# Kernel optimization log

Hardware: AMD Instinct MI355X
Metric: run time of the kernel (lower is better)

The kernel has to match this reference:

```python
import jax, jax.numpy as jnp
import numpy as np

D_IN, D_OUT, RANK, N = 4096, 4096, 16, 8192


def _quantize_weight(w, bits):
    # round-to-nearest fake quantization, stored back as floats (as in the torch code)
    absmax = jnp.abs(w).max()
    scale = (2 ** (bits - 1) - 1) / absmax
    q = jnp.clip(jnp.round(w * scale), -2 ** (bits - 1), 2 ** (bits - 1) - 1)
    return q / scale


def _double_quantization(w, bits):
    absmax = jnp.abs(w).max()
    c1 = (2 ** (bits - 1) - 1) / absmax          # scalar fp32 scale
    q = jnp.clip(jnp.round(w * c1), -2 ** (bits - 1), 2 ** (bits - 1) - 1)
    return c1, q / c1                             # c_kbit_2 has same shape as w


def setup_inputs() -> dict:
    key = jax.random.key(0)
    kX, kW, kL1, kL2 = jax.random.split(key, 4)
    X = jax.random.normal(kX, (N, D_IN), dtype=jnp.float32)
    W0 = jax.random.normal(kW, (D_IN, D_OUT), dtype=jnp.float32)
    W_nf4 = _quantize_weight(W0, bits=4)
    c_fp32_1, c_kbit_2 = _double_quantization(W_nf4, bits=8)
    L1 = jax.random.normal(kL1, (D_IN, RANK), dtype=jnp.float32)
    L2 = jax.random.normal(kL2, (RANK, D_OUT), dtype=jnp.float32)
    return {"X": X, "W_nf4": W_nf4, "c_fp32_1": c_fp32_1,
            "c_kbit_2": c_kbit_2, "L1": L1, "L2": L2}


def reference(X, W_nf4, c_fp32_1, c_kbit_2, L1, L2):
    # dequantize: elementwise scalar * elementwise-tensor scaling of stored weight
    W = W_nf4 * c_fp32_1 * c_kbit_2               # [D_IN, D_OUT]
    # main GEMM + low-rank LoRA path, added in the epilogue
    Y = X @ W + (X @ L1) @ L2                     # [N, D_OUT]
    return Y
```

## Files before the change

kernel.cpp:

```cpp
#include <hip/hip_runtime.h>


#define M_ROWS 8192
#define K_DIM  4096
#define N_OUT  4096

typedef float  f32x4  __attribute__((ext_vector_type(4)));
typedef __bf16 bf16x8 __attribute__((ext_vector_type(8)));
typedef unsigned short ushort8v __attribute__((ext_vector_type(8)));

__device__ __forceinline__ unsigned short f2bf(float f) {
    __bf16 h = (__bf16)f;
    union { __bf16 h; unsigned short u; } v; v.h = h;
    return v.u;
}

__global__ __launch_bounds__(256) void cvt_x_kernel(const float* __restrict__ X,
                                                    ushort8v* __restrict__ Xh) {
    size_t tid = (size_t)blockIdx.x * 256 + threadIdx.x;
    const float4* xp = (const float4*)X;
    float4 a = xp[tid * 2];
    float4 b = xp[tid * 2 + 1];
    ushort8v o;
    o[0] = f2bf(a.x); o[1] = f2bf(a.y); o[2] = f2bf(a.z); o[3] = f2bf(a.w);
    o[4] = f2bf(b.x); o[5] = f2bf(b.y); o[6] = f2bf(b.z); o[7] = f2bf(b.w);
    Xh[tid] = o;
}

__global__ __launch_bounds__(256) void prep_w_kernel(
        const float* __restrict__ Wnf4, const float* __restrict__ c1p,
        const float* __restrict__ c2,   const float* __restrict__ L1,
        const float* __restrict__ L2,   unsigned short* __restrict__ Wt) {
    __shared__ float tile[64][65];
    __shared__ float sL2[16][64];
    __shared__ float sL1[64][16];
    const int t  = threadIdx.x;
    const int n0 = blockIdx.x * 64;
    const int k0 = blockIdx.y * 64;
    const float c1 = *c1p;

    {
        int r = t >> 4, c4 = (t & 15) * 4;
        *(float4*)&sL2[r][c4] = *(const float4*)&L2[(size_t)r * N_OUT + n0 + c4];
        int r1 = t >> 2, c1v = (t & 3) * 4;
        *(float4*)&sL1[r1][c1v] = *(const float4*)&L1[(size_t)(k0 + r1) * 16 + c1v];
    }
    __syncthreads();

    #pragma unroll
    for (int i = 0; i < 4; ++i) {
        int idx = i * 1024 + t * 4;
        int kk = idx >> 6, nn = idx & 63;
        size_t g = (size_t)(k0 + kk) * N_OUT + n0 + nn;
        float4 w = *(const float4*)&Wnf4[g];
        float4 s = *(const float4*)&c2[g];
        float o0 = w.x * c1 * s.x, o1 = w.y * c1 * s.y;
        float o2 = w.z * c1 * s.z, o3 = w.w * c1 * s.w;
        #pragma unroll
        for (int r = 0; r < 16; ++r) {
            float a = sL1[kk][r];
            o0 += a * sL2[r][nn];     o1 += a * sL2[r][nn + 1];
            o2 += a * sL2[r][nn + 2]; o3 += a * sL2[r][nn + 3];
        }
        tile[kk][nn] = o0; tile[kk][nn + 1] = o1;
        tile[kk][nn + 2] = o2; tile[kk][nn + 3] = o3;
    }
    __syncthreads();

    #pragma unroll
    for (int i = 0; i < 2; ++i) {
        int task = i * 256 + t;
        int kg = task & 7, nn = task >> 3;
        ushort8v o;
        #pragma unroll
        for (int j = 0; j < 8; ++j) o[j] = f2bf(tile[kg * 8 + j][nn]);
        *(ushort8v*)&Wt[(size_t)(n0 + nn) * K_DIM + k0 + kg * 8] = o;
    }
}

__global__ __launch_bounds__(256) void gemm_bt_kernel(
        const __bf16* __restrict__ A, const __bf16* __restrict__ Bt,
        float* __restrict__ C) {
    __shared__ __bf16 As[128 * 32];
    __shared__ __bf16 Bs[128 * 32];

    const int t    = threadIdx.x;
    const int w    = t >> 6;
    const int lane = t & 63;
    const int quad = lane >> 4;
    const int l16  = lane & 15;
    const int m0   = blockIdx.y * 128;
    const int n0   = blockIdx.x * 128;
    const int wm   = (w >> 1) * 64;
    const int wn   = (w & 1) * 64;

    const int srow = lane >> 2;
    const int scol = ((lane & 3) ^ ((lane >> 3) & 3)) * 8;
    const int rsw = (l16 >> 1) & 3;

    f32x4 acc[4][4] = {};

    for (int kb = 0; kb < K_DIM; kb += 32) {
        __syncthreads();
        #pragma unroll
        for (int j = 0; j < 2; ++j) {
            int row = w * 32 + j * 16 + srow;
            const __bf16* gp = A + (size_t)(m0 + row) * K_DIM + kb + scol;
            __builtin_amdgcn_global_load_lds(
                (const __attribute__((address_space(1))) unsigned int*)gp,
                (__attribute__((address_space(3))) unsigned int*)(As + (w * 32 + j * 16) * 32),
                16, 0, 0);
        }
        #pragma unroll
        for (int j = 0; j < 2; ++j) {
            int row = w * 32 + j * 16 + srow;
            const __bf16* gp = Bt + (size_t)(n0 + row) * K_DIM + kb + scol;
            __builtin_amdgcn_global_load_lds(
                (const __attribute__((address_space(1))) unsigned int*)gp,
                (__attribute__((address_space(3))) unsigned int*)(Bs + (w * 32 + j * 16) * 32),
                16, 0, 0);
        }
        __syncthreads();

        bf16x8 af[4], bf[4];
        #pragma unroll
        for (int i = 0; i < 4; ++i)
            af[i] = *(const bf16x8*)(As + (wm + i * 16 + l16) * 32 + ((quad ^ rsw) * 8));
        #pragma unroll
        for (int i = 0; i < 4; ++i)
            bf[i] = *(const bf16x8*)(Bs + (wn + i * 16 + l16) * 32 + ((quad ^ rsw) * 8));

        #pragma unroll
        for (int mt = 0; mt < 4; ++mt)
            #pragma unroll
            for (int nt = 0; nt < 4; ++nt)
                acc[mt][nt] = __builtin_amdgcn_mfma_f32_16x16x32_bf16(
                    af[mt], bf[nt], acc[mt][nt], 0, 0, 0);
    }

    #pragma unroll
    for (int mt = 0; mt < 4; ++mt) {
        int row = m0 + wm + mt * 16 + quad * 4;
        #pragma unroll
        for (int nt = 0; nt < 4; ++nt) {
            int col = n0 + wn + nt * 16 + l16;
            float* cp = C + (size_t)row * N_OUT + col;
            #pragma unroll
            for (int r = 0; r < 4; ++r)
                cp[(size_t)r * N_OUT] = acc[mt][nt][r];
        }
    }
}

extern "C" void kernel_launch(void* const* d_in, const int* in_sizes, int n_in,
                              void* d_out, int out_size, void* d_ws, size_t ws_size,
                              hipStream_t stream) {
    const float* X    = (const float*)d_in[0];
    const float* Wnf4 = (const float*)d_in[1];
    const float* c1   = (const float*)d_in[2];
    const float* c2   = (const float*)d_in[3];
    const float* L1   = (const float*)d_in[4];
    const float* L2   = (const float*)d_in[5];
    float* Y = (float*)d_out;

    unsigned short* Xh = (unsigned short*)d_ws;
    unsigned short* Wt = (unsigned short*)((char*)d_ws + (size_t)M_ROWS * K_DIM * 2);

    cvt_x_kernel<<<(M_ROWS * K_DIM / 8 + 255) / 256, 256, 0, stream>>>(X, (ushort8v*)Xh);
    prep_w_kernel<<<dim3(N_OUT / 64, K_DIM / 64), 256, 0, stream>>>(Wnf4, c1, c2, L1, L2, Wt);
    gemm_bt_kernel<<<dim3(N_OUT / 128, M_ROWS / 128), 256, 0, stream>>>(
        (const __bf16*)Xh, (const __bf16*)Wt, Y);
}
```

Baseline: 737.0 us.

## Switch GEMM to 32x32x16 MFMA tiles and merge prep kernels into one launch

The GEMM inner loop now issues 32x32x16 bf16 MFMAs on 2x2 accumulator tiles per wave instead of 16x16x32 MFMAs on 4x4 tiles. The fragment loads from shared memory and the output row mapping are rewritten to match. Separately, the X conversion and weight preparation kernels are merged into one launch that picks its branch by block index. The intent is fewer MFMA issues and LDS reads per k-step and one less kernel launch, at the cost of a larger per-instruction latency and a more scattered epilogue store pattern.

```diff
diff --git a/kernel.cpp b/kernel.cpp
--- a/kernel.cpp
+++ b/kernel.cpp
@@ -4,8 +4,10 @@
 #define M_ROWS 8192
 #define K_DIM  4096
 #define N_OUT  4096
+#define CVT_BLOCKS 16384
+#define PREPW_BLOCKS 4096
 
-typedef float  f32x4  __attribute__((ext_vector_type(4)));
+typedef float  f32x16 __attribute__((ext_vector_type(16)));
 typedef __bf16 bf16x8 __attribute__((ext_vector_type(8)));
 typedef unsigned short ushort8v __attribute__((ext_vector_type(8)));
 
@@ -15,28 +17,31 @@
     return v.u;
 }
 
-__global__ __launch_bounds__(256) void cvt_x_kernel(const float* __restrict__ X,
-                                                    ushort8v* __restrict__ Xh) {
-    size_t tid = (size_t)blockIdx.x * 256 + threadIdx.x;
-    const float4* xp = (const float4*)X;
-    float4 a = xp[tid * 2];
-    float4 b = xp[tid * 2 + 1];
-    ushort8v o;
-    o[0] = f2bf(a.x); o[1] = f2bf(a.y); o[2] = f2bf(a.z); o[3] = f2bf(a.w);
-    o[4] = f2bf(b.x); o[5] = f2bf(b.y); o[6] = f2bf(b.z); o[7] = f2bf(b.w);
-    Xh[tid] = o;
-}
-
-__global__ __launch_bounds__(256) void prep_w_kernel(
+__global__ __launch_bounds__(256) void prep_kernel(
+        const float* __restrict__ X,    ushort8v* __restrict__ Xh,
         const float* __restrict__ Wnf4, const float* __restrict__ c1p,
         const float* __restrict__ c2,   const float* __restrict__ L1,
         const float* __restrict__ L2,   unsigned short* __restrict__ Wt) {
     __shared__ float tile[64][65];
     __shared__ float sL2[16][64];
     __shared__ float sL1[64][16];
-    const int t  = threadIdx.x;
-    const int n0 = blockIdx.x * 64;
-    const int k0 = blockIdx.y * 64;
+    const int t = threadIdx.x;
+
+    if (blockIdx.x < CVT_BLOCKS) {
+        size_t tid = (size_t)blockIdx.x * 256 + t;
+        const float4* xp = (const float4*)X;
+        float4 a = xp[tid * 2];
+        float4 b = xp[tid * 2 + 1];
+        ushort8v o;
+        o[0] = f2bf(a.x); o[1] = f2bf(a.y); o[2] = f2bf(a.z); o[3] = f2bf(a.w);
+        o[4] = f2bf(b.x); o[5] = f2bf(b.y); o[6] = f2bf(b.z); o[7] = f2bf(b.w);
+        Xh[tid] = o;
+        return;
+    }
+
+    const int wb = blockIdx.x - CVT_BLOCKS;
+    const int n0 = (wb & 63) * 64;
+    const int k0 = (wb >> 6) * 64;
     const float c1 = *c1p;
 
     {
@@ -87,8 +92,8 @@
     const int t    = threadIdx.x;
     const int w    = t >> 6;
     const int lane = t & 63;
-    const int quad = lane >> 4;
-    const int l16  = lane & 15;
+    const int half = lane >> 5;
+    const int l32  = lane & 31;
     const int m0   = blockIdx.y * 128;
     const int n0   = blockIdx.x * 128;
     const int wm   = (w >> 1) * 64;
@@ -96,9 +101,9 @@
 
     const int srow = lane >> 2;
     const int scol = ((lane & 3) ^ ((lane >> 3) & 3)) * 8;
-    const int rsw = (l16 >> 1) & 3;
+    const int rsw = (l32 >> 1) & 3;
 
-    f32x4 acc[4][4] = {};
+    f32x16 acc[2][2] = {};
 
     for (int kb = 0; kb < K_DIM; kb += 32) {
         __syncthreads();
@@ -122,34 +127,45 @@
         }
         __syncthreads();
 
-        bf16x8 af[4], bf[4];
+        bf16x8 af[2][2], bf[2][2];
         #pragma unroll
-        for (int i = 0; i < 4; ++i)
-            af[i] = *(const bf16x8*)(As + (wm + i * 16 + l16) * 32 + ((quad ^ rsw) * 8));
+        for (int mt = 0; mt < 2; ++mt)
+            #pragma unroll
+            for (int ks = 0; ks < 2; ++ks) {
+                int row = wm + mt * 32 + l32;
+                int slot = (2 * ks + half) ^ rsw;
+                af[mt][ks] = *(const bf16x8*)(As + row * 32 + slot * 8);
+            }
         #pragma unroll
-        for (int i = 0; i < 4; ++i)
-            bf[i] = *(const bf16x8*)(Bs + (wn + i * 16 + l16) * 32 + ((quad ^ rsw) * 8));
+        for (int nt = 0; nt < 2; ++nt)
+            #pragma unroll
+            for (int ks = 0; ks < 2; ++ks) {
+                int row = wn + nt * 32 + l32;
+                int slot = (2 * ks + half) ^ rsw;
+                bf[nt][ks] = *(const bf16x8*)(Bs + row * 32 + slot * 8);
+            }
 
         #pragma unroll
-        for (int mt = 0; mt < 4; ++mt)
+        for (int ks = 0; ks < 2; ++ks)
             #pragma unroll
-            for (int nt = 0; nt < 4; ++nt)
-                acc[mt][nt] = __builtin_amdgcn_mfma_f32_16x16x32_bf16(
-                    af[mt], bf[nt], acc[mt][nt], 0, 0, 0);
+            for (int mt = 0; mt < 2; ++mt)
+                #pragma unroll
+                for (int nt = 0; nt < 2; ++nt)
+                    acc[mt][nt] = __builtin_amdgcn_mfma_f32_32x32x16_bf16(
+                        af[mt][ks], bf[nt][ks], acc[mt][nt], 0, 0, 0);
     }
 
     #pragma unroll
-    for (int mt = 0; mt < 4; ++mt) {
-        int row = m0 + wm + mt * 16 + quad * 4;
+    for (int mt = 0; mt < 2; ++mt)
         #pragma unroll
-        for (int nt = 0; nt < 4; ++nt) {
-            int col = n0 + wn + nt * 16 + l16;
-            float* cp = C + (size_t)row * N_OUT + col;
+        for (int nt = 0; nt < 2; ++nt) {
+            int col = n0 + wn + nt * 32 + l32;
             #pragma unroll
-            for (int r = 0; r < 4; ++r)
-                cp[(size_t)r * N_OUT] = acc[mt][nt][r];
+            for (int reg = 0; reg < 16; ++reg) {
+                int row = m0 + wm + mt * 32 + (reg & 3) + 8 * (reg >> 2) + 4 * half;
+                C[(size_t)row * N_OUT + col] = acc[mt][nt][reg];
+            }
         }
-    }
 }
 
 extern "C" void kernel_launch(void* const* d_in, const int* in_sizes, int n_in,
@@ -166,8 +182,8 @@
     unsigned short* Xh = (unsigned short*)d_ws;
     unsigned short* Wt = (unsigned short*)((char*)d_ws + (size_t)M_ROWS * K_DIM * 2);
 
-    cvt_x_kernel<<<(M_ROWS * K_DIM / 8 + 255) / 256, 256, 0, stream>>>(X, (ushort8v*)Xh);
-    prep_w_kernel<<<dim3(N_OUT / 64, K_DIM / 64), 256, 0, stream>>>(Wnf4, c1, c2, L1, L2, Wt);
+    prep_kernel<<<CVT_BLOCKS + PREPW_BLOCKS, 256, 0, stream>>>(
+        X, (ushort8v*)Xh, Wnf4, c1, c2, L1, L2, Wt);
     gemm_bt_kernel<<<dim3(N_OUT / 128, M_ROWS / 128), 256, 0, stream>>>(
         (const __bf16*)Xh, (const __bf16*)Wt, Y);
 }
```

Result: faster. 641.8 us (-12.9%).
